# Performance work log

Measured on AMD Instinct MI355X. Metric: run time of the kernel, lower is better.

## Reference

```python
import jax, jax.numpy as jnp
import numpy as np

EMBED_DIM = 512
K = 30
B, M, L = 64, 1024, 256

def setup_inputs() -> dict:
    key = jax.random.key(0)
    ks = jax.random.split(key, 7)
    s = 0.05  # small scale so tanh/softmax stay in a sane numeric range
    return {
        "V": jax.random.normal(ks[0], (B, EMBED_DIM, M), dtype=jnp.float32),
        "Q": jax.random.normal(ks[1], (B, L, EMBED_DIM), dtype=jnp.float32),
        "W_b": jax.random.normal(ks[2], (EMBED_DIM, EMBED_DIM), dtype=jnp.float32) * s,
        "W_v": jax.random.normal(ks[3], (K, EMBED_DIM), dtype=jnp.float32) * s,
        "W_q": jax.random.normal(ks[4], (K, EMBED_DIM), dtype=jnp.float32) * s,
        "w_hv": jax.random.normal(ks[5], (K, 1), dtype=jnp.float32) * s,
        "w_hq": jax.random.normal(ks[6], (K, 1), dtype=jnp.float32) * s,
    }

def reference(V, Q, W_b, W_v, W_q, w_hv, w_hq):
    # V: [B, d, M], Q: [B, L, d]
    b, d, m = V.shape
    l = Q.shape[1]
    WbV = jnp.einsum('de,bem->bdm', W_b, V)          # [B, d, M]
    C = jnp.matmul(Q, WbV)                            # affinity [B, L, M]
    WvV = jnp.einsum('kd,bdm->bkm', W_v, V)           # [B, k, M]
    WqQ = jnp.einsum('kd,bld->bkl', W_q, Q)           # [B, k, L]
    H_v = jnp.tanh(WvV + jnp.matmul(WqQ, C))          # [B, k, M]
    H_q = jnp.tanh(WqQ + jnp.matmul(WvV, jnp.swapaxes(C, 1, 2)))  # [B, k, L]
    a_v = jax.nn.softmax(jnp.einsum('ko,bkm->bom', w_hv, H_v), axis=2)  # [B, 1, M]
    a_q = jax.nn.softmax(jnp.einsum('ko,bkl->bol', w_hq, H_q), axis=2)  # [B, 1, L]
    # torch stacks a_v M times then matmuls -> M identical pooled rows; compute
    # the pooled vector once and broadcast (same math, no [B,M,M] intermediate).
    v1 = jnp.matmul(a_v, jnp.swapaxes(V, 1, 2))       # [B, 1, d]
    q1 = jnp.matmul(a_q, Q)                           # [B, 1, d]
    v = jnp.broadcast_to(v1, (b, m, d))               # [B, M, d]
    q = jnp.broadcast_to(q1, (b, l, d))               # [B, L, d]
    return (v, q)
```

## Files before the change

### kernel.cpp

```cpp
#include <hip/hip_runtime.h>

constexpr int Bn = 64;
constexpr int Dn = 512;
constexpr int Mn = 1024;
constexpr int Ln = 256;
constexpr int Kn = 30;
constexpr int KP = 32;

typedef __attribute__((ext_vector_type(4))) float f32x4;
typedef __attribute__((ext_vector_type(2))) float f32x2;
typedef __attribute__((ext_vector_type(4))) unsigned int u32x4;
typedef __attribute__((ext_vector_type(2))) unsigned int u32x2;
typedef __attribute__((ext_vector_type(8))) _Float16 f16x8;
typedef __attribute__((ext_vector_type(2))) _Float16 f16x2;
typedef unsigned short ushort_t;

__device__ __forceinline__ unsigned int cvt_one_pack(float x)
{
    _Float16 h = (_Float16)x;
    _Float16 l = (_Float16)(x - (float)h);
    return (unsigned int)__builtin_bit_cast(ushort_t, l) |
           ((unsigned int)__builtin_bit_cast(ushort_t, h) << 16);
}

__device__ __forceinline__ float unpacksplit(unsigned int p)
{
    _Float16 h = __builtin_bit_cast(_Float16, (ushort_t)(p >> 16));
    _Float16 l = __builtin_bit_cast(_Float16, (ushort_t)(p & 0xffffu));
    return (float)h + (float)l;
}

__device__ __forceinline__ void cvt_pair(float a, float b,
                                         unsigned int& hp, unsigned int& lp)
{
    _Float16 ha = (_Float16)a, hb = (_Float16)b;
    _Float16 la = (_Float16)(a - (float)ha), lb = (_Float16)(b - (float)hb);
    f16x2 hv = {ha, hb}, lv = {la, lb};
    hp = __builtin_bit_cast(unsigned int, hv);
    lp = __builtin_bit_cast(unsigned int, lv);
}

#define PERM_HI 0x07060302u
#define PERM_LO 0x05040100u

__global__ __launch_bounds__(256) void pack4_kernel(
    const float* __restrict__ s0, unsigned int* __restrict__ d0, long n0,
    const float* __restrict__ s1, unsigned int* __restrict__ d1, long n1,
    const float* __restrict__ s2, unsigned int* __restrict__ d2, long n2,
    const float* __restrict__ s3, unsigned int* __restrict__ d3, long n3)
{
    long total4 = (n0 + n1 + n2 + n3) >> 2;
    long stride = (long)gridDim.x * blockDim.x;
    for (long c = (long)blockIdx.x * blockDim.x + threadIdx.x; c < total4; c += stride) {
        long i = c * 4;
        const float* s; unsigned int* d; long off;
        if (i < n0)                { s = s0; d = d0; off = i; }
        else if (i < n0 + n1)      { s = s1; d = d1; off = i - n0; }
        else if (i < n0 + n1 + n2) { s = s2; d = d2; off = i - n0 - n1; }
        else                       { s = s3; d = d3; off = i - n0 - n1 - n2; }
        f32x4 v = *(const f32x4*)(s + off);
        u32x4 o = { cvt_one_pack(v.x), cvt_one_pack(v.y),
                    cvt_one_pack(v.z), cvt_one_pack(v.w) };
        *(u32x4*)(d + off) = o;
    }
}

template <int MT, bool BT, int EPI, bool BPACK, int ASRC>
__global__ __launch_bounds__(256) void fgemm_kernel(
    const unsigned int* __restrict__ A, const void* __restrict__ B,
    const unsigned int* __restrict__ A2,
    unsigned int* __restrict__ C,
    const float* __restrict__ Wvec, const unsigned int* __restrict__ Xadd,
    float* __restrict__ Yout,
    int Mreal, int Ndim, int Kdim, int ldA, int ldB,
    long sA, long sB, long sC)
{
    constexpr int BM = MT * 16;
    constexpr int AP = 20;
    constexpr int ASZ = BM * AP;
    constexpr int BP_NN = 66;
    constexpr int BSZ = BT ? (2 * 64 * AP) : (32 * BP_NN);
    constexpr int HALF = 2 * ASZ + BSZ;
    __shared__ unsigned int smem[2 * HALF];
    __shared__ float wsh[32];

    const int t  = threadIdx.x;
    const int n0 = blockIdx.x * 64;
    const int m0 = blockIdx.y * BM;
    const int b  = blockIdx.z;
    const unsigned int* Ab = A + (long)b * sA;
    const float*        Bf = (const float*)B + (long)b * sB;
    const unsigned int* Bu = (const unsigned int*)B + (long)b * sB;

    const int lane = t & 63, w = t >> 6;
    const int fr = lane & 15, g = lane >> 4;
    const int kp  = t & 15, r16 = t >> 4;
    const int nn  = t & 63, kr  = t >> 6;

    if (EPI >= 2 && t < 32) wsh[t] = (t < Kn) ? Wvec[t] : 0.f;

    unsigned int aA[MT][2];
    unsigned int bu[8];
    float bf[8];

    auto stageA = [&](int k0) {
        #pragma unroll
        for (int i = 0; i < MT; i++) {
            int gm = m0 + r16 + 16 * i;
            unsigned int p0 = 0, p1 = 0;
            if constexpr (ASRC == 2) {
                if (gm < Kn) {
                    u32x2 v = *(const u32x2*)&A[(long)gm * ldA + k0 + 2 * kp];
                    p0 = v.x; p1 = v.y;
                } else if (gm >= 32) {
                    u32x2 v = *(const u32x2*)&A2[((long)b * 32 + gm - 32) * ldA + k0 + 2 * kp];
                    p0 = v.x; p1 = v.y;
                }
            } else {
                if (gm < Mreal) {
                    u32x2 v = *(const u32x2*)&Ab[(long)gm * ldA + k0 + 2 * kp];
                    p0 = v.x; p1 = v.y;
                }
            }
            aA[i][0] = p0; aA[i][1] = p1;
        }
    };
    auto stageB = [&](int k0) {
        if constexpr (BT) {
            #pragma unroll
            for (int i = 0; i < 4; i++) {
                long off = (long)(n0 + r16 + 16 * i) * ldB + k0 + 2 * kp;
                if constexpr (BPACK) {
                    u32x2 v = *(const u32x2*)&Bu[off];
                    bu[2 * i] = v.x; bu[2 * i + 1] = v.y;
                } else {
                    f32x2 v = *(const f32x2*)&Bf[off];
                    bf[2 * i] = v.x; bf[2 * i + 1] = v.y;
                }
            }
        } else {
            #pragma unroll
            for (int i = 0; i < 8; i++) {
                long off = (long)(k0 + kr + 4 * i) * ldB + n0 + nn;
                if constexpr (BPACK) bu[i] = Bu[off];
                else                 bf[i] = Bf[off];
            }
        }
    };
    auto storeStage = [&](unsigned int* sm) {
        unsigned int* Ah = sm;
        unsigned int* Al = sm + ASZ;
        #pragma unroll
        for (int i = 0; i < MT; i++) {
            Ah[(r16 + 16 * i) * AP + kp] = __builtin_amdgcn_perm(aA[i][1], aA[i][0], PERM_HI);
            Al[(r16 + 16 * i) * AP + kp] = __builtin_amdgcn_perm(aA[i][1], aA[i][0], PERM_LO);
        }
        if constexpr (BT) {
            unsigned int* Bh = sm + 2 * ASZ;
            unsigned int* Bl = Bh + 64 * AP;
            #pragma unroll
            for (int i = 0; i < 4; i++) {
                unsigned int hp, lp;
                if constexpr (BPACK) {
                    hp = __builtin_amdgcn_perm(bu[2 * i + 1], bu[2 * i], PERM_HI);
                    lp = __builtin_amdgcn_perm(bu[2 * i + 1], bu[2 * i], PERM_LO);
                } else {
                    cvt_pair(bf[2 * i], bf[2 * i + 1], hp, lp);
                }
                Bh[(r16 + 16 * i) * AP + kp] = hp;
                Bl[(r16 + 16 * i) * AP + kp] = lp;
            }
        } else {
            unsigned int* Bp = sm + 2 * ASZ;
            #pragma unroll
            for (int i = 0; i < 8; i++)
                Bp[(kr + 4 * i) * BP_NN + nn] = BPACK ? bu[i] : cvt_one_pack(bf[i]);
        }
    };

    f32x4 acc[MT];
    #pragma unroll
    for (int i = 0; i < MT; i++) acc[i] = (f32x4){0.f, 0.f, 0.f, 0.f};

    auto computeTile = [&](const unsigned int* sm) {
        const unsigned int* Ah = sm;
        const unsigned int* Al = sm + ASZ;
        f16x8 fbh, fbl;
        if constexpr (BT) {
            const unsigned int* Bh = sm + 2 * ASZ;
            const unsigned int* Bl = Bh + 64 * AP;
            int row = w * 16 + fr;
            fbh = __builtin_bit_cast(f16x8, *(const u32x4*)&Bh[row * AP + g * 4]);
            fbl = __builtin_bit_cast(f16x8, *(const u32x4*)&Bl[row * AP + g * 4]);
        } else {
            const unsigned int* Bp = sm + 2 * ASZ;
            unsigned int p[8];
            #pragma unroll
            for (int j = 0; j < 8; j++)
                p[j] = Bp[(g * 8 + j) * BP_NN + w * 16 + fr];
            unsigned int hu[4], lu[4];
            #pragma unroll
            for (int r = 0; r < 4; r++) {
                hu[r] = __builtin_amdgcn_perm(p[2 * r + 1], p[2 * r], PERM_HI);
                lu[r] = __builtin_amdgcn_perm(p[2 * r + 1], p[2 * r], PERM_LO);
            }
            fbh = __builtin_bit_cast(f16x8, (u32x4){hu[0], hu[1], hu[2], hu[3]});
            fbl = __builtin_bit_cast(f16x8, (u32x4){lu[0], lu[1], lu[2], lu[3]});
        }
        #pragma unroll
        for (int mt = 0; mt < MT; mt++) {
            int row = fr + 16 * mt;
            f16x8 fah = __builtin_bit_cast(f16x8, *(const u32x4*)&Ah[row * AP + g * 4]);
            f16x8 fal = __builtin_bit_cast(f16x8, *(const u32x4*)&Al[row * AP + g * 4]);
            acc[mt] = __builtin_amdgcn_mfma_f32_16x16x32_f16(fah, fbh, acc[mt], 0, 0, 0);
            acc[mt] = __builtin_amdgcn_mfma_f32_16x16x32_f16(fal, fbh, acc[mt], 0, 0, 0);
            acc[mt] = __builtin_amdgcn_mfma_f32_16x16x32_f16(fah, fbl, acc[mt], 0, 0, 0);
        }
    };

    const int nt = Kdim >> 5;
    stageA(0); stageB(0);
    storeStage(smem);
    __syncthreads();
    for (int tt = 0; tt < nt; tt++) {
        unsigned int* cur = smem + (tt & 1) * HALF;
        unsigned int* nxt = smem + ((tt + 1) & 1) * HALF;
        const bool more = (tt + 1 < nt);
        if (more) { stageA((tt + 1) << 5); stageB((tt + 1) << 5); }
        computeTile(cur);
        if (more) storeStage(nxt);
        __syncthreads();
    }

    const int col = n0 + w * 16 + fr;
    if constexpr (EPI == 0) {
        unsigned int* Cb = C + (long)b * sC;
        #pragma unroll
        for (int mt = 0; mt < MT; mt++)
            #pragma unroll
            for (int r = 0; r < 4; r++)
                Cb[(long)(m0 + mt * 16 + g * 4 + r) * Ndim + col] = cvt_one_pack(acc[mt][r]);
    } else if constexpr (EPI == 2) {
        unsigned int* Cb = C + (long)b * sC;
        float s = 0.f;
        #pragma unroll
        for (int mt = 0; mt < 2; mt++)
            #pragma unroll
            for (int r = 0; r < 4; r++) {
                int row = mt * 16 + g * 4 + r;
                Cb[(long)row * Ndim + col] = cvt_one_pack(acc[mt][r]);
                s += wsh[row] * tanhf(acc[mt][r] + acc[mt + 2][r]);
            }
        s += __shfl_xor(s, 16, 64);
        s += __shfl_xor(s, 32, 64);
        if (g == 0) Yout[(long)b * Ndim + col] = s;
    } else {
        const unsigned int* Xb = Xadd + (long)b * sC;
        float s = 0.f;
        #pragma unroll
        for (int mt = 0; mt < MT; mt++)
            #pragma unroll
            for (int r = 0; r < 4; r++) {
                int row = mt * 16 + g * 4 + r;
                float x = unpacksplit(Xb[(long)row * Ndim + col]);
                s += wsh[row] * tanhf(x + acc[mt][r]);
            }
        s += __shfl_xor(s, 16, 64);
        s += __shfl_xor(s, 32, 64);
        if (g == 0) Yout[(long)b * Ndim + col] = s;
    }
}

__global__ __launch_bounds__(1024) void smpool_v_kernel(
    const float* __restrict__ sv, const float* __restrict__ V,
    float* __restrict__ v1)
{
    const int b = blockIdx.y, qtr = blockIdx.x, t = threadIdx.x;
    const int wid = t >> 6, lane = t & 63;
    __shared__ float red[16];
    __shared__ float bc;
    __shared__ float av[Mn];

    float x = sv[(long)b * Mn + t];
    float v = x;
    #pragma unroll
    for (int off = 32; off > 0; off >>= 1) v = fmaxf(v, __shfl_down(v, off, 64));
    if (lane == 0) red[wid] = v;
    __syncthreads();
    if (t == 0) {
        float m = red[0];
        for (int i = 1; i < 16; i++) m = fmaxf(m, red[i]);
        bc = m;
    }
    __syncthreads();
    float e = expf(x - bc);
    v = e;
    #pragma unroll
    for (int off = 32; off > 0; off >>= 1) v += __shfl_down(v, off, 64);
    if (lane == 0) red[wid] = v;
    __syncthreads();
    if (t == 0) {
        float s = 0.f;
        for (int i = 0; i < 16; i++) s += red[i];
        bc = s;
    }
    __syncthreads();
    av[t] = e / bc;
    __syncthreads();

    f32x4 aa[4];
    #pragma unroll
    for (int i = 0; i < 4; i++) aa[i] = *(const f32x4*)&av[4 * (lane + 64 * i)];

    #pragma unroll
    for (int j = 0; j < 8; j++) {
        int e_ = qtr * 128 + wid * 8 + j;
        const float* vr = V + ((long)b * Dn + e_) * Mn;
        float acc = 0.f;
        #pragma unroll
        for (int i = 0; i < 4; i++) {
            f32x4 vv = *(const f32x4*)&vr[4 * (lane + 64 * i)];
            acc += vv.x * aa[i].x + vv.y * aa[i].y + vv.z * aa[i].z + vv.w * aa[i].w;
        }
        #pragma unroll
        for (int off = 32; off > 0; off >>= 1) acc += __shfl_down(acc, off, 64);
        if (lane == 0) v1[(long)b * Dn + e_] = acc;
    }
}

__global__ __launch_bounds__(256) void smpool_q_kernel(
    const float* __restrict__ sq, const float* __restrict__ Q,
    float* __restrict__ q1)
{
    const int b = blockIdx.y, eb = blockIdx.x, t = threadIdx.x;
    const int wid = t >> 6, lane = t & 63;
    __shared__ float red[4];
    __shared__ float bc;
    __shared__ float aq[Ln];

    float x = sq[(long)b * Ln + t];
    float v = x;
    #pragma unroll
    for (int off = 32; off > 0; off >>= 1) v = fmaxf(v, __shfl_down(v, off, 64));
    if (lane == 0) red[wid] = v;
    __syncthreads();
    if (t == 0) {
        float m = red[0];
        for (int i = 1; i < 4; i++) m = fmaxf(m, red[i]);
        bc = m;
    }
    __syncthreads();
    float e = expf(x - bc);
    v = e;
    #pragma unroll
    for (int off = 32; off > 0; off >>= 1) v += __shfl_down(v, off, 64);
    if (lane == 0) red[wid] = v;
    __syncthreads();
    if (t == 0) {
        float s = 0.f;
        for (int i = 0; i < 4; i++) s += red[i];
        bc = s;
    }
    __syncthreads();
    aq[t] = e / bc;
    __syncthreads();

    const int e_ = eb * 64 + (t >> 2), qtr = t & 3;
    const float* Qb = Q + (long)b * Ln * Dn;
    float acc = 0.f;
    #pragma unroll 4
    for (int i = 0; i < 64; i++) {
        int l = qtr * 64 + i;
        acc += aq[l] * Qb[(long)l * Dn + e_];
    }
    acc += __shfl_xor(acc, 1, 64);
    acc += __shfl_xor(acc, 2, 64);
    if (qtr == 0) q1[(long)b * Dn + e_] = acc;
}

__global__ void bcast_kernel(const float* __restrict__ v1,
                             const float* __restrict__ q1,
                             float* __restrict__ out)
{
    const long nv4 = (long)Bn * Mn * Dn / 4;
    const long nq4 = (long)Bn * Ln * Dn / 4;
    long idx = (long)blockIdx.x * blockDim.x + threadIdx.x;
    float4* o4 = (float4*)out;
    if (idx < nv4) {
        long fidx = idx * 4;
        int e4 = (int)(fidx & (Dn - 1));
        long bm = fidx >> 9;
        int b = (int)(bm >> 10);
        o4[idx] = *(const float4*)(v1 + (long)b * Dn + e4);
    } else if (idx < nv4 + nq4) {
        long fidx = (idx - nv4) * 4;
        int e4 = (int)(fidx & (Dn - 1));
        long bl = fidx >> 9;
        int b = (int)(bl >> 8);
        o4[idx] = *(const float4*)(q1 + (long)b * Dn + e4);
    }
}


extern "C" void kernel_launch(void* const* d_in, const int* in_sizes, int n_in,
                              void* d_out, int out_size, void* d_ws, size_t ws_size,
                              hipStream_t stream)
{
    const float* V    = (const float*)d_in[0];
    const float* Q    = (const float*)d_in[1];
    const float* W_b  = (const float*)d_in[2];
    const float* W_v  = (const float*)d_in[3];
    const float* W_q  = (const float*)d_in[4];
    const float* w_hv = (const float*)d_in[5];
    const float* w_hq = (const float*)d_in[6];
    float* out = (float*)d_out;

    const long nQ  = (long)Bn * Ln * Dn;
    const long nWb = (long)Dn * Dn;
    const long nWq = (long)Kn * Dn;
    const long nWv = (long)Kn * Dn;
    const long szWqQ = (long)Bn * KP * Ln;
    const long szU   = (long)Bn * KP * Dn;
    const long szSo  = (long)Bn * KP * Mn;

    unsigned int* wsu   = (unsigned int*)d_ws;
    unsigned int* Qp    = wsu;
    unsigned int* Wbp   = Qp    + nQ;
    unsigned int* Wqp   = Wbp   + nWb;
    unsigned int* Wvp   = Wqp   + nWq;
    unsigned int* WqQp  = Wvp   + nWv;
    unsigned int* Up    = WqQp  + szWqQ;
    unsigned int* Pp    = Up    + szU;
    unsigned int* Soutp = Pp    + szU;
    unsigned int* Rp    = Soutp + szSo;
    unsigned int* Gp    = Rp    + szU;
    float* sv = (float*)(Gp + szU);
    float* sq = sv + (long)Bn * Mn;
    float* v1 = sq + (long)Bn * Ln;
    float* q1 = v1 + (long)Bn * Dn;

    pack4_kernel<<<4096, 256, 0, stream>>>(
        Q, Qp, nQ, W_b, Wbp, nWb, W_q, Wqp, nWq, W_v, Wvp, nWv);

    fgemm_kernel<2, true, 0, true, 0><<<dim3(4, 1, 64), 256, 0, stream>>>(
        Wqp, Qp, nullptr, WqQp, nullptr, nullptr, nullptr,
        Kn, Ln, Dn, Dn, Dn, 0, (long)Ln * Dn, (long)KP * Ln);

    fgemm_kernel<2, false, 0, true, 0><<<dim3(8, 1, 64), 256, 0, stream>>>(
        WqQp, Qp, nullptr, Up, nullptr, nullptr, nullptr,
        KP, Dn, Ln, Ln, Dn, (long)KP * Ln, (long)Ln * Dn, (long)KP * Dn);

    fgemm_kernel<4, false, 0, true, 0><<<dim3(8, 32, 1), 256, 0, stream>>>(
        Up, Wbp, nullptr, Pp, nullptr, nullptr, nullptr,
        Bn * KP, Dn, Dn, Dn, Dn, 0, 0, 0);

    fgemm_kernel<4, false, 2, false, 2><<<dim3(16, 1, 64), 256, 0, stream>>>(
        Wvp, V, Pp, Soutp, w_hv, nullptr, sv,
        64, Mn, Dn, Dn, Mn, 0, (long)Dn * Mn, (long)KP * Mn);

    fgemm_kernel<2, true, 0, false, 0><<<dim3(8, 1, 64), 256, 0, stream>>>(
        Soutp, V, nullptr, Rp, nullptr, nullptr, nullptr,
        KP, Dn, Mn, Mn, Mn, (long)KP * Mn, (long)Dn * Mn, (long)KP * Dn);

    fgemm_kernel<4, true, 0, true, 0><<<dim3(8, 32, 1), 256, 0, stream>>>(
        Rp, Wbp, nullptr, Gp, nullptr, nullptr, nullptr,
        Bn * KP, Dn, Dn, Dn, Dn, 0, 0, 0);

    fgemm_kernel<2, true, 3, true, 0><<<dim3(4, 1, 64), 256, 0, stream>>>(
        Gp, Qp, nullptr, nullptr, w_hq, WqQp, sq,
        KP, Ln, Dn, Dn, Dn, (long)KP * Dn, (long)Ln * Dn, (long)KP * Ln);

    smpool_v_kernel<<<dim3(4, Bn), 1024, 0, stream>>>(sv, V, v1);
    smpool_q_kernel<<<dim3(8, Bn), 256, 0, stream>>>(sq, Q, q1);

    {
        long n4 = (long)Bn * Mn * Dn / 4 + (long)Bn * Ln * Dn / 4;
        bcast_kernel<<<(int)((n4 + 255) / 256), 256, 0, stream>>>(v1, q1, out);
    }
}
```

Baseline: 451.8 us.

## Drop pre-pack kernel, fuse softmax-pool with broadcast write, co-schedule with GEMM

Removes the separate pack kernel that split Q, W_b, W_q and W_v into hi/lo fp16 pairs, and instead converts fp32 operands on the fly while staging each GEMM tile. The v-side softmax pooling is fused with the broadcast store and runs as extra blocks inside the same launch as the Soutp×V GEMM. The q-side pooling writes its broadcast output directly, so the standalone bcast kernel is gone. The two W_b GEMMs use a smaller M tile with twice the grid. This cuts the extra passes over Q and the output and lowers launch count, at the cost of repeated conversion work and rereading fp32 operands inside the GEMMs.

```diff
diff --git a/kernel.cpp b/kernel.cpp
--- a/kernel.cpp
+++ b/kernel.cpp
@@ -43,54 +43,34 @@
 #define PERM_HI 0x07060302u
 #define PERM_LO 0x05040100u
 
-__global__ __launch_bounds__(256) void pack4_kernel(
-    const float* __restrict__ s0, unsigned int* __restrict__ d0, long n0,
-    const float* __restrict__ s1, unsigned int* __restrict__ d1, long n1,
-    const float* __restrict__ s2, unsigned int* __restrict__ d2, long n2,
-    const float* __restrict__ s3, unsigned int* __restrict__ d3, long n3)
-{
-    long total4 = (n0 + n1 + n2 + n3) >> 2;
-    long stride = (long)gridDim.x * blockDim.x;
-    for (long c = (long)blockIdx.x * blockDim.x + threadIdx.x; c < total4; c += stride) {
-        long i = c * 4;
-        const float* s; unsigned int* d; long off;
-        if (i < n0)                { s = s0; d = d0; off = i; }
-        else if (i < n0 + n1)      { s = s1; d = d1; off = i - n0; }
-        else if (i < n0 + n1 + n2) { s = s2; d = d2; off = i - n0 - n1; }
-        else                       { s = s3; d = d3; off = i - n0 - n1 - n2; }
-        f32x4 v = *(const f32x4*)(s + off);
-        u32x4 o = { cvt_one_pack(v.x), cvt_one_pack(v.y),
-                    cvt_one_pack(v.z), cvt_one_pack(v.w) };
-        *(u32x4*)(d + off) = o;
-    }
-}
-
-template <int MT, bool BT, int EPI, bool BPACK, int ASRC>
-__global__ __launch_bounds__(256) void fgemm_kernel(
-    const unsigned int* __restrict__ A, const void* __restrict__ B,
-    const unsigned int* __restrict__ A2,
-    unsigned int* __restrict__ C,
-    const float* __restrict__ Wvec, const unsigned int* __restrict__ Xadd,
-    float* __restrict__ Yout,
+template <int MT, bool BT> struct LdsCfg {
+    static constexpr int AP    = 20;
+    static constexpr int ASZ   = MT * 16 * AP;
+    static constexpr int BP_NN = 66;
+    static constexpr int BSZ   = BT ? (2 * 64 * AP) : (32 * BP_NN);
+    static constexpr int HALF  = 2 * ASZ + BSZ;
+    static constexpr int TOT   = 2 * HALF + 32;
+};
+
+template <int MT, bool BT, int EPI, bool AF32, int ASRC>
+__device__ __forceinline__ void fgemm_dev(
+    unsigned int* smem, int nb, int mb, int b,
+    const void* Av, const float* B, const unsigned int* A2,
+    unsigned int* C, const float* Wvec, const unsigned int* Xadd,
+    float* Yout,
     int Mreal, int Ndim, int Kdim, int ldA, int ldB,
     long sA, long sB, long sC)
 {
-    constexpr int BM = MT * 16;
-    constexpr int AP = 20;
-    constexpr int ASZ = BM * AP;
-    constexpr int BP_NN = 66;
-    constexpr int BSZ = BT ? (2 * 64 * AP) : (32 * BP_NN);
-    constexpr int HALF = 2 * ASZ + BSZ;
-    __shared__ unsigned int smem[2 * HALF];
-    __shared__ float wsh[32];
+    using L = LdsCfg<MT, BT>;
+    constexpr int AP = L::AP, ASZ = L::ASZ, BP_NN = L::BP_NN, HALF = L::HALF;
+    float* wsh = (float*)(smem + 2 * HALF);
 
     const int t  = threadIdx.x;
-    const int n0 = blockIdx.x * 64;
-    const int m0 = blockIdx.y * BM;
-    const int b  = blockIdx.z;
-    const unsigned int* Ab = A + (long)b * sA;
-    const float*        Bf = (const float*)B + (long)b * sB;
-    const unsigned int* Bu = (const unsigned int*)B + (long)b * sB;
+    const int n0 = nb * 64;
+    const int m0 = mb * MT * 16;
+    const float*        Afb = (const float*)Av + (long)b * sA;
+    const unsigned int* Aub = (const unsigned int*)Av + (long)b * sA;
+    const float*        Bb  = B + (long)b * sB;
 
     const int lane = t & 63, w = t >> 6;
     const int fr = lane & 15, g = lane >> 4;
@@ -99,52 +79,52 @@
 
     if (EPI >= 2 && t < 32) wsh[t] = (t < Kn) ? Wvec[t] : 0.f;
 
+    float asf[MT][2];
     unsigned int aA[MT][2];
-    unsigned int bu[8];
     float bf[8];
 
     auto stageA = [&](int k0) {
         #pragma unroll
         for (int i = 0; i < MT; i++) {
             int gm = m0 + r16 + 16 * i;
-            unsigned int p0 = 0, p1 = 0;
             if constexpr (ASRC == 2) {
                 if (gm < Kn) {
-                    u32x2 v = *(const u32x2*)&A[(long)gm * ldA + k0 + 2 * kp];
-                    p0 = v.x; p1 = v.y;
+                    f32x2 v = *(const f32x2*)&((const float*)Av)[(long)gm * ldA + k0 + 2 * kp];
+                    asf[i][0] = v.x; asf[i][1] = v.y;
                 } else if (gm >= 32) {
                     u32x2 v = *(const u32x2*)&A2[((long)b * 32 + gm - 32) * ldA + k0 + 2 * kp];
+                    aA[i][0] = v.x; aA[i][1] = v.y;
+                } else {
+                    asf[i][0] = 0.f; asf[i][1] = 0.f;
+                }
+            } else if constexpr (AF32) {
+                float x0 = 0.f, x1 = 0.f;
+                if (gm < Mreal) {
+                    f32x2 v = *(const f32x2*)&Afb[(long)gm * ldA + k0 + 2 * kp];
+                    x0 = v.x; x1 = v.y;
+                }
+                asf[i][0] = x0; asf[i][1] = x1;
+            } else {
+                unsigned int p0 = 0, p1 = 0;
+                if (gm < Mreal) {
+                    u32x2 v = *(const u32x2*)&Aub[(long)gm * ldA + k0 + 2 * kp];
                     p0 = v.x; p1 = v.y;
                 }
-            } else {
-                if (gm < Mreal) {
-                    u32x2 v = *(const u32x2*)&Ab[(long)gm * ldA + k0 + 2 * kp];
-                    p0 = v.x; p1 = v.y;
-                }
-            }
-            aA[i][0] = p0; aA[i][1] = p1;
+                aA[i][0] = p0; aA[i][1] = p1;
+            }
         }
     };
     auto stageB = [&](int k0) {
         if constexpr (BT) {
             #pragma unroll
             for (int i = 0; i < 4; i++) {
-                long off = (long)(n0 + r16 + 16 * i) * ldB + k0 + 2 * kp;
-                if constexpr (BPACK) {
-                    u32x2 v = *(const u32x2*)&Bu[off];
-                    bu[2 * i] = v.x; bu[2 * i + 1] = v.y;
-                } else {
-                    f32x2 v = *(const f32x2*)&Bf[off];
-                    bf[2 * i] = v.x; bf[2 * i + 1] = v.y;
-                }
+                f32x2 v = *(const f32x2*)&Bb[(long)(n0 + r16 + 16 * i) * ldB + k0 + 2 * kp];
+                bf[2 * i] = v.x; bf[2 * i + 1] = v.y;
             }
         } else {
             #pragma unroll
-            for (int i = 0; i < 8; i++) {
-                long off = (long)(k0 + kr + 4 * i) * ldB + n0 + nn;
-                if constexpr (BPACK) bu[i] = Bu[off];
-                else                 bf[i] = Bf[off];
-            }
+            for (int i = 0; i < 8; i++)
+                bf[i] = Bb[(long)(k0 + kr + 4 * i) * ldB + n0 + nn];
         }
     };
     auto storeStage = [&](unsigned int* sm) {
@@ -152,8 +132,22 @@
         unsigned int* Al = sm + ASZ;
         #pragma unroll
         for (int i = 0; i < MT; i++) {
-            Ah[(r16 + 16 * i) * AP + kp] = __builtin_amdgcn_perm(aA[i][1], aA[i][0], PERM_HI);
-            Al[(r16 + 16 * i) * AP + kp] = __builtin_amdgcn_perm(aA[i][1], aA[i][0], PERM_LO);
+            unsigned int hp, lp;
+            if constexpr (ASRC == 2) {
+                int gm = m0 + r16 + 16 * i;
+                if (gm < 32) cvt_pair(asf[i][0], asf[i][1], hp, lp);
+                else {
+                    hp = __builtin_amdgcn_perm(aA[i][1], aA[i][0], PERM_HI);
+                    lp = __builtin_amdgcn_perm(aA[i][1], aA[i][0], PERM_LO);
+                }
+            } else if constexpr (AF32) {
+                cvt_pair(asf[i][0], asf[i][1], hp, lp);
+            } else {
+                hp = __builtin_amdgcn_perm(aA[i][1], aA[i][0], PERM_HI);
+                lp = __builtin_amdgcn_perm(aA[i][1], aA[i][0], PERM_LO);
+            }
+            Ah[(r16 + 16 * i) * AP + kp] = hp;
+            Al[(r16 + 16 * i) * AP + kp] = lp;
         }
         if constexpr (BT) {
             unsigned int* Bh = sm + 2 * ASZ;
@@ -161,12 +155,7 @@
             #pragma unroll
             for (int i = 0; i < 4; i++) {
                 unsigned int hp, lp;
-                if constexpr (BPACK) {
-                    hp = __builtin_amdgcn_perm(bu[2 * i + 1], bu[2 * i], PERM_HI);
-                    lp = __builtin_amdgcn_perm(bu[2 * i + 1], bu[2 * i], PERM_LO);
-                } else {
-                    cvt_pair(bf[2 * i], bf[2 * i + 1], hp, lp);
-                }
+                cvt_pair(bf[2 * i], bf[2 * i + 1], hp, lp);
                 Bh[(r16 + 16 * i) * AP + kp] = hp;
                 Bl[(r16 + 16 * i) * AP + kp] = lp;
             }
@@ -174,7 +163,7 @@
             unsigned int* Bp = sm + 2 * ASZ;
             #pragma unroll
             for (int i = 0; i < 8; i++)
-                Bp[(kr + 4 * i) * BP_NN + nn] = BPACK ? bu[i] : cvt_one_pack(bf[i]);
+                Bp[(kr + 4 * i) * BP_NN + nn] = cvt_one_pack(bf[i]);
         }
     };
 
@@ -271,133 +260,147 @@
     }
 }
 
-__global__ __launch_bounds__(1024) void smpool_v_kernel(
+template <int MT, bool BT, int EPI, bool AF32, int ASRC>
+__global__ __launch_bounds__(256) void fgemm_kernel(
+    const void* A, const float* B, const unsigned int* A2,
+    unsigned int* C, const float* Wvec, const unsigned int* Xadd,
+    float* Yout,
+    int Mreal, int Ndim, int Kdim, int ldA, int ldB,
+    long sA, long sB, long sC)
+{
+    __shared__ unsigned int smem[LdsCfg<MT, BT>::TOT];
+    fgemm_dev<MT, BT, EPI, AF32, ASRC>(smem, blockIdx.x, blockIdx.y, blockIdx.z,
+        A, B, A2, C, Wvec, Xadd, Yout, Mreal, Ndim, Kdim, ldA, ldB, sA, sB, sC);
+}
+
+__device__ __forceinline__ void smv_body(float* sm, int eb, int b,
     const float* __restrict__ sv, const float* __restrict__ V,
-    float* __restrict__ v1)
-{
-    const int b = blockIdx.y, qtr = blockIdx.x, t = threadIdx.x;
-    const int wid = t >> 6, lane = t & 63;
-    __shared__ float red[16];
-    __shared__ float bc;
-    __shared__ float av[Mn];
-
-    float x = sv[(long)b * Mn + t];
-    float v = x;
-    #pragma unroll
-    for (int off = 32; off > 0; off >>= 1) v = fmaxf(v, __shfl_down(v, off, 64));
-    if (lane == 0) red[wid] = v;
-    __syncthreads();
-    if (t == 0) {
-        float m = red[0];
-        for (int i = 1; i < 16; i++) m = fmaxf(m, red[i]);
-        bc = m;
-    }
-    __syncthreads();
-    float e = expf(x - bc);
-    v = e;
-    #pragma unroll
-    for (int off = 32; off > 0; off >>= 1) v += __shfl_down(v, off, 64);
-    if (lane == 0) red[wid] = v;
-    __syncthreads();
-    if (t == 0) {
-        float s = 0.f;
-        for (int i = 0; i < 16; i++) s += red[i];
-        bc = s;
-    }
-    __syncthreads();
-    av[t] = e / bc;
-    __syncthreads();
+    float* __restrict__ outv)
+{
+    float* av  = sm;
+    float* ev  = sm + 1024;
+    float* red = sm + 1088;
+    float* bcp = sm + 1092;
+    const int t = threadIdx.x, lane = t & 63, w = t >> 6;
+    const int e0 = eb * 64;
+
+    f32x4 x4 = *(const f32x4*)&sv[(long)b * Mn + 4 * t];
+    float mx = fmaxf(fmaxf(x4.x, x4.y), fmaxf(x4.z, x4.w));
+    #pragma unroll
+    for (int off = 32; off > 0; off >>= 1) mx = fmaxf(mx, __shfl_down(mx, off, 64));
+    if (lane == 0) red[w] = mx;
+    __syncthreads();
+    if (t == 0) bcp[0] = fmaxf(fmaxf(red[0], red[1]), fmaxf(red[2], red[3]));
+    __syncthreads();
+    const float m = bcp[0];
+    f32x4 e4 = {expf(x4.x - m), expf(x4.y - m), expf(x4.z - m), expf(x4.w - m)};
+    *(f32x4*)&av[4 * t] = e4;
+    float se = e4.x + e4.y + e4.z + e4.w;
+    #pragma unroll
+    for (int off = 32; off > 0; off >>= 1) se += __shfl_down(se, off, 64);
+    if (lane == 0) red[w] = se;
+    __syncthreads();
+    if (t == 0) bcp[0] = 1.f / (red[0] + red[1] + red[2] + red[3]);
+    __syncthreads();
+    const float rinv = bcp[0];
 
     f32x4 aa[4];
     #pragma unroll
     for (int i = 0; i < 4; i++) aa[i] = *(const f32x4*)&av[4 * (lane + 64 * i)];
 
-    #pragma unroll
-    for (int j = 0; j < 8; j++) {
-        int e_ = qtr * 128 + wid * 8 + j;
-        const float* vr = V + ((long)b * Dn + e_) * Mn;
+    for (int i = 0; i < 16; i++) {
+        int el = w * 16 + i;
+        const float* vr = V + ((long)b * Dn + e0 + el) * Mn;
         float acc = 0.f;
         #pragma unroll
-        for (int i = 0; i < 4; i++) {
-            f32x4 vv = *(const f32x4*)&vr[4 * (lane + 64 * i)];
-            acc += vv.x * aa[i].x + vv.y * aa[i].y + vv.z * aa[i].z + vv.w * aa[i].w;
+        for (int s = 0; s < 4; s++) {
+            f32x4 v4 = *(const f32x4*)&vr[4 * (lane + 64 * s)];
+            acc += v4.x * aa[s].x + v4.y * aa[s].y + v4.z * aa[s].z + v4.w * aa[s].w;
         }
         #pragma unroll
         for (int off = 32; off > 0; off >>= 1) acc += __shfl_down(acc, off, 64);
-        if (lane == 0) v1[(long)b * Dn + e_] = acc;
-    }
-}
-
-__global__ __launch_bounds__(256) void smpool_q_kernel(
+        if (lane == 0) ev[el] = acc * rinv;
+    }
+    __syncthreads();
+
+    const int c4 = t & 15;
+    f32x4 ev4 = ((const f32x4*)ev)[c4];
+    #pragma unroll 4
+    for (int rep = 0; rep < 64; rep++) {
+        int row = rep * 16 + (t >> 4);
+        *(f32x4*)&outv[((long)b * Mn + row) * Dn + e0 + 4 * c4] = ev4;
+    }
+}
+
+__global__ __launch_bounds__(256) void g7smv_kernel(
+    const unsigned int* __restrict__ Soutp, const float* __restrict__ V,
+    unsigned int* __restrict__ Rp, const float* __restrict__ sv,
+    float* __restrict__ outv)
+{
+    constexpr int TOT = LdsCfg<2, true>::TOT;
+    __shared__ unsigned int smem[TOT];
+    if (blockIdx.x < 8) {
+        fgemm_dev<2, true, 0, false, 0>(smem, blockIdx.x, 0, blockIdx.z,
+            Soutp, V, nullptr, Rp, nullptr, nullptr, nullptr,
+            KP, Dn, Mn, Mn, Mn,
+            (long)KP * Mn, (long)Dn * Mn, (long)KP * Dn);
+    } else {
+        smv_body((float*)smem, blockIdx.x - 8, blockIdx.z, sv, V, outv);
+    }
+}
+
+__global__ __launch_bounds__(256) void smq_out_kernel(
     const float* __restrict__ sq, const float* __restrict__ Q,
-    float* __restrict__ q1)
-{
+    float* __restrict__ outq)
+{
+    __shared__ float sm[326];
+    float* aq  = sm;
+    float* ev  = sm + 256;
+    float* red = sm + 320;
+    float* bcp = sm + 324;
     const int b = blockIdx.y, eb = blockIdx.x, t = threadIdx.x;
-    const int wid = t >> 6, lane = t & 63;
-    __shared__ float red[4];
-    __shared__ float bc;
-    __shared__ float aq[Ln];
+    const int lane = t & 63, w = t >> 6;
+    const int e0 = eb * 64;
 
     float x = sq[(long)b * Ln + t];
-    float v = x;
-    #pragma unroll
-    for (int off = 32; off > 0; off >>= 1) v = fmaxf(v, __shfl_down(v, off, 64));
-    if (lane == 0) red[wid] = v;
-    __syncthreads();
-    if (t == 0) {
-        float m = red[0];
-        for (int i = 1; i < 4; i++) m = fmaxf(m, red[i]);
-        bc = m;
-    }
-    __syncthreads();
-    float e = expf(x - bc);
-    v = e;
-    #pragma unroll
-    for (int off = 32; off > 0; off >>= 1) v += __shfl_down(v, off, 64);
-    if (lane == 0) red[wid] = v;
-    __syncthreads();
-    if (t == 0) {
-        float s = 0.f;
-        for (int i = 0; i < 4; i++) s += red[i];
-        bc = s;
-    }
-    __syncthreads();
-    aq[t] = e / bc;
-    __syncthreads();
-
-    const int e_ = eb * 64 + (t >> 2), qtr = t & 3;
+    float mx = x;
+    #pragma unroll
+    for (int off = 32; off > 0; off >>= 1) mx = fmaxf(mx, __shfl_down(mx, off, 64));
+    if (lane == 0) red[w] = mx;
+    __syncthreads();
+    if (t == 0) bcp[0] = fmaxf(fmaxf(red[0], red[1]), fmaxf(red[2], red[3]));
+    __syncthreads();
+    const float m = bcp[0];
+    float e = expf(x - m);
+    aq[t] = e;
+    float se = e;
+    #pragma unroll
+    for (int off = 32; off > 0; off >>= 1) se += __shfl_down(se, off, 64);
+    if (lane == 0) red[w] = se;
+    __syncthreads();
+    if (t == 0) bcp[0] = 1.f / (red[0] + red[1] + red[2] + red[3]);
+    __syncthreads();
+    const float rinv = bcp[0];
+
+    const int e_l = t >> 2, qtr = t & 3;
     const float* Qb = Q + (long)b * Ln * Dn;
     float acc = 0.f;
     #pragma unroll 4
     for (int i = 0; i < 64; i++) {
         int l = qtr * 64 + i;
-        acc += aq[l] * Qb[(long)l * Dn + e_];
+        acc += aq[l] * Qb[(long)l * Dn + e0 + e_l];
     }
     acc += __shfl_xor(acc, 1, 64);
     acc += __shfl_xor(acc, 2, 64);
-    if (qtr == 0) q1[(long)b * Dn + e_] = acc;
-}
-
-__global__ void bcast_kernel(const float* __restrict__ v1,
-                             const float* __restrict__ q1,
-                             float* __restrict__ out)
-{
-    const long nv4 = (long)Bn * Mn * Dn / 4;
-    const long nq4 = (long)Bn * Ln * Dn / 4;
-    long idx = (long)blockIdx.x * blockDim.x + threadIdx.x;
-    float4* o4 = (float4*)out;
-    if (idx < nv4) {
-        long fidx = idx * 4;
-        int e4 = (int)(fidx & (Dn - 1));
-        long bm = fidx >> 9;
-        int b = (int)(bm >> 10);
-        o4[idx] = *(const float4*)(v1 + (long)b * Dn + e4);
-    } else if (idx < nv4 + nq4) {
-        long fidx = (idx - nv4) * 4;
-        int e4 = (int)(fidx & (Dn - 1));
-        long bl = fidx >> 9;
-        int b = (int)(bl >> 8);
-        o4[idx] = *(const float4*)(q1 + (long)b * Dn + e4);
+    if (qtr == 0) ev[e_l] = acc * rinv;
+    __syncthreads();
+
+    const int c4 = t & 15;
+    f32x4 ev4 = ((const f32x4*)ev)[c4];
+    #pragma unroll 4
+    for (int rep = 0; rep < 16; rep++) {
+        int row = rep * 16 + (t >> 4);
+        *(f32x4*)&outq[((long)b * Ln + row) * Dn + e0 + 4 * c4] = ev4;
     }
 }
 
@@ -415,20 +418,12 @@
     const float* w_hq = (const float*)d_in[6];
     float* out = (float*)d_out;
 
-    const long nQ  = (long)Bn * Ln * Dn;
-    const long nWb = (long)Dn * Dn;
-    const long nWq = (long)Kn * Dn;
-    const long nWv = (long)Kn * Dn;
     const long szWqQ = (long)Bn * KP * Ln;
     const long szU   = (long)Bn * KP * Dn;
     const long szSo  = (long)Bn * KP * Mn;
 
     unsigned int* wsu   = (unsigned int*)d_ws;
-    unsigned int* Qp    = wsu;
-    unsigned int* Wbp   = Qp    + nQ;
-    unsigned int* Wqp   = Wbp   + nWb;
-    unsigned int* Wvp   = Wqp   + nWq;
-    unsigned int* WqQp  = Wvp   + nWv;
+    unsigned int* WqQp  = wsu;
     unsigned int* Up    = WqQp  + szWqQ;
     unsigned int* Pp    = Up    + szU;
     unsigned int* Soutp = Pp    + szU;
@@ -436,45 +431,35 @@
     unsigned int* Gp    = Rp    + szU;
     float* sv = (float*)(Gp + szU);
     float* sq = sv + (long)Bn * Mn;
-    float* v1 = sq + (long)Bn * Ln;
-    float* q1 = v1 + (long)Bn * Dn;
-
-    pack4_kernel<<<4096, 256, 0, stream>>>(
-        Q, Qp, nQ, W_b, Wbp, nWb, W_q, Wqp, nWq, W_v, Wvp, nWv);
+
+    float* outv = out;
+    float* outq = out + (long)Bn * Mn * Dn;
 
     fgemm_kernel<2, true, 0, true, 0><<<dim3(4, 1, 64), 256, 0, stream>>>(
-        Wqp, Qp, nullptr, WqQp, nullptr, nullptr, nullptr,
+        W_q, Q, nullptr, WqQp, nullptr, nullptr, nullptr,
         Kn, Ln, Dn, Dn, Dn, 0, (long)Ln * Dn, (long)KP * Ln);
 
-    fgemm_kernel<2, false, 0, true, 0><<<dim3(8, 1, 64), 256, 0, stream>>>(
-        WqQp, Qp, nullptr, Up, nullptr, nullptr, nullptr,
+    fgemm_kernel<2, false, 0, false, 0><<<dim3(8, 1, 64), 256, 0, stream>>>(
+        WqQp, Q, nullptr, Up, nullptr, nullptr, nullptr,
         KP, Dn, Ln, Ln, Dn, (long)KP * Ln, (long)Ln * Dn, (long)KP * Dn);
 
-    fgemm_kernel<4, false, 0, true, 0><<<dim3(8, 32, 1), 256, 0, stream>>>(
-        Up, Wbp, nullptr, Pp, nullptr, nullptr, nullptr,
+    fgemm_kernel<2, false, 0, false, 0><<<dim3(8, 64, 1), 256, 0, stream>>>(
+        Up, W_b, nullptr, Pp, nullptr, nullptr, nullptr,
         Bn * KP, Dn, Dn, Dn, Dn, 0, 0, 0);
 
-    fgemm_kernel<4, false, 2, false, 2><<<dim3(16, 1, 64), 256, 0, stream>>>(
-        Wvp, V, Pp, Soutp, w_hv, nullptr, sv,
+    fgemm_kernel<4, false, 2, true, 2><<<dim3(16, 1, 64), 256, 0, stream>>>(
+        W_v, V, Pp, Soutp, w_hv, nullptr, sv,
         64, Mn, Dn, Dn, Mn, 0, (long)Dn * Mn, (long)KP * Mn);
 
-    fgemm_kernel<2, true, 0, false, 0><<<dim3(8, 1, 64), 256, 0, stream>>>(
-        Soutp, V, nullptr, Rp, nullptr, nullptr, nullptr,
-        KP, Dn, Mn, Mn, Mn, (long)KP * Mn, (long)Dn * Mn, (long)KP * Dn);
-
-    fgemm_kernel<4, true, 0, true, 0><<<dim3(8, 32, 1), 256, 0, stream>>>(
-        Rp, Wbp, nullptr, Gp, nullptr, nullptr, nullptr,
+    g7smv_kernel<<<dim3(16, 1, 64), 256, 0, stream>>>(Soutp, V, Rp, sv, outv);
+
+    fgemm_kernel<2, true, 0, false, 0><<<dim3(8, 64, 1), 256, 0, stream>>>(
+        Rp, W_b, nullptr, Gp, nullptr, nullptr, nullptr,
         Bn * KP, Dn, Dn, Dn, Dn, 0, 0, 0);
 
-    fgemm_kernel<2, true, 3, true, 0><<<dim3(4, 1, 64), 256, 0, stream>>>(
-        Gp, Qp, nullptr, nullptr, w_hq, WqQp, sq,
+    fgemm_kernel<2, true, 3, false, 0><<<dim3(4, 1, 64), 256, 0, stream>>>(
+        Gp, Q, nullptr, nullptr, w_hq, WqQp, sq,
         KP, Ln, Dn, Dn, Dn, (long)KP * Dn, (long)Ln * Dn, (long)KP * Ln);
 
-    smpool_v_kernel<<<dim3(4, Bn), 1024, 0, stream>>>(sv, V, v1);
-    smpool_q_kernel<<<dim3(8, Bn), 256, 0, stream>>>(sq, Q, q1);
-
-    {
-        long n4 = (long)Bn * Mn * Dn / 4 + (long)Bn * Ln * Dn / 4;
-        bcast_kernel<<<(int)((n4 + 255) / 256), 256, 0, stream>>>(v1, q1, out);
-    }
-}
+    smq_out_kernel<<<dim3(8, Bn), 256, 0, stream>>>(sq, Q, outq);
+}
```

Measured after the change: 448.1 us. About the same (-0.8%).
